# Kernel tuning notes

Hardware: AMD Instinct MI355X
Metric: run time of the kernel (lower is better)

The kernel has to match this reference:

```python
import jax, jax.numpy as jnp
import numpy as np

N, IN_CH, OUT_CH = 100000, 512, 512


def setup_inputs() -> dict:
    key = jax.random.key(0)
    k1, k2, k3, k4 = jax.random.split(key, 4)
    # Xavier-uniform bounds: sqrt(6/(fan_in+fan_out)); Im uses gain=0.1
    bound = float(np.sqrt(6.0 / (IN_CH + OUT_CH)))
    x_re = jax.random.normal(k1, (N, IN_CH), dtype=jnp.float32)
    x_im = jax.random.normal(k2, (N, IN_CH), dtype=jnp.float32)
    Re = jax.random.uniform(k3, (OUT_CH, IN_CH), dtype=jnp.float32, minval=-bound, maxval=bound)
    Im = jax.random.uniform(k4, (OUT_CH, IN_CH), dtype=jnp.float32, minval=-0.1 * bound, maxval=0.1 * bound)
    return {"x_re": x_re, "x_im": x_im, "Re": Re, "Im": Im}


def reference(x_re, x_im, Re, Im):
    # Complex linear: out = x @ (Re + i*Im)^T, summed over in_channels.
    # Equivalent to torch.sum(x[:,None,:] * W[None,:,:], dim=2) but as GEMMs.
    out_re = jnp.einsum('ni,oi->no', x_re, Re) - jnp.einsum('ni,oi->no', x_im, Im)
    out_im = jnp.einsum('ni,oi->no', x_re, Im) + jnp.einsum('ni,oi->no', x_im, Re)
    return jnp.stack([out_re, out_im])  # (2, N, out_channels): real, imag
```

## Files before the change

### kernel.cpp

```cpp
#include <hip/hip_runtime.h>
#include <hip/hip_bf16.h>
#include <cstdint>

#define NROWS  100000
#define KDIM   1024
#define MPAD   100096
#define MTILES 391
#define NTILES 4
#define NBLK   (MTILES * NTILES)

typedef __attribute__((ext_vector_type(8))) __bf16 bf16x8;
typedef __attribute__((ext_vector_type(4))) float  f32x4;

__device__ __forceinline__ uint16_t f2bf(float f) {
    union { float f; uint32_t u; } v; v.f = f;
    uint32_t u = v.u;
    u += 0x7FFFu + ((u >> 16) & 1u);
    return (uint16_t)(u >> 16);
}

__device__ __forceinline__ void async16(const uint16_t* g, uint16_t* l) {
    __builtin_amdgcn_global_load_lds(
        (const __attribute__((address_space(1))) uint32_t*)g,
        (__attribute__((address_space(3))) uint32_t*)l,
        16, 0, 0);
}

__global__ __launch_bounds__(256) void pack_a_kernel(
        const float* __restrict__ xre, const float* __restrict__ xim,
        uint16_t* __restrict__ A) {
    int c = blockIdx.x * 256 + threadIdx.x;
    int n = c >> 7;
    int j = c & 127;
    uint32_t p0 = 0, p1 = 0, p2 = 0, p3 = 0;
    if (n < NROWS) {
        const float* src = (j < 64) ? (xre + (size_t)n * 512 + (size_t)j * 8)
                                    : (xim + (size_t)n * 512 + (size_t)(j - 64) * 8);
        float4 a = ((const float4*)src)[0];
        float4 b = ((const float4*)src)[1];
        p0 = (uint32_t)f2bf(a.x) | ((uint32_t)f2bf(a.y) << 16);
        p1 = (uint32_t)f2bf(a.z) | ((uint32_t)f2bf(a.w) << 16);
        p2 = (uint32_t)f2bf(b.x) | ((uint32_t)f2bf(b.y) << 16);
        p3 = (uint32_t)f2bf(b.z) | ((uint32_t)f2bf(b.w) << 16);
    }
    uint4 v; v.x = p0; v.y = p1; v.z = p2; v.w = p3;
    *(uint4*)(A + (size_t)c * 8) = v;
}

__global__ __launch_bounds__(256) void pack_b_kernel(
        const float* __restrict__ Re, const float* __restrict__ Im,
        uint16_t* __restrict__ Bt) {
    int c  = blockIdx.x * 256 + threadIdx.x;
    int oc = c >> 7;
    int j  = c & 127;
    const float* src;
    float sgn = 1.0f;
    if (oc < 512) {
        if (j < 64) { src = Re + (size_t)oc * 512 + (size_t)j * 8; }
        else        { src = Im + (size_t)oc * 512 + (size_t)(j - 64) * 8; sgn = -1.0f; }
    } else {
        int o = oc - 512;
        if (j < 64) { src = Im + (size_t)o * 512 + (size_t)j * 8; }
        else        { src = Re + (size_t)o * 512 + (size_t)(j - 64) * 8; }
    }
    float4 a = ((const float4*)src)[0];
    float4 b = ((const float4*)src)[1];
    uint32_t p0 = (uint32_t)f2bf(sgn * a.x) | ((uint32_t)f2bf(sgn * a.y) << 16);
    uint32_t p1 = (uint32_t)f2bf(sgn * a.z) | ((uint32_t)f2bf(sgn * a.w) << 16);
    uint32_t p2 = (uint32_t)f2bf(sgn * b.x) | ((uint32_t)f2bf(sgn * b.y) << 16);
    uint32_t p3 = (uint32_t)f2bf(sgn * b.z) | ((uint32_t)f2bf(sgn * b.w) << 16);
    uint4 v; v.x = p0; v.y = p1; v.z = p2; v.w = p3;
    *(uint4*)(Bt + (size_t)c * 8) = v;
}

__global__ __launch_bounds__(512, 2) void gemm8(
        const uint16_t* __restrict__ A, const uint16_t* __restrict__ Bt,
        float* __restrict__ C) {
    __shared__ uint16_t lds[65536];

    const int t    = threadIdx.x;
    const int wave = t >> 6;
    const int lane = t & 63;
    const int q    = lane >> 4;
    const int r16  = lane & 15;
    const int wm   = wave >> 2;
    const int wn   = wave & 3;

    const int bid  = blockIdx.x;
    const int xcd  = bid & 7, lid = bid >> 3;
    const int wgid = (xcd < 4 ? xcd * 196 : 784 + (xcd - 4) * 195) + lid;
    const int colTile = wgid & 3;
    const int rowTile = wgid >> 2;
    const int aRow0   = rowTile * 256;

    const int s7  = r16 & 7;
    const int sA0 = r16 * 64 + ((q ^ s7) << 3);
    const int sA1 = r16 * 64 + (((q + 4) ^ s7) << 3);

    const int g0 = t, g1 = t + 512;
    const int r0 = g0 >> 3, k0 = ((g0 & 7) ^ (r0 & 7)) << 3;
    const int r1 = g1 >> 3, k1 = ((g1 & 7) ^ (r1 & 7)) << 3;
    const int lA00 = g0 * 8,          lA01 = g1 * 8;
    const int lA10 = 8192 + g0 * 8,   lA11 = 8192 + g1 * 8;
    const int lB00 = 16384 + g0 * 8,  lB01 = 16384 + g1 * 8;
    const int lB10 = 24576 + g0 * 8,  lB11 = 24576 + g1 * 8;
    const uint16_t* pA00 = A  + (size_t)(aRow0 + r0) * KDIM + k0;
    const uint16_t* pA01 = A  + (size_t)(aRow0 + r1) * KDIM + k1;
    const uint16_t* pA10 = A  + (size_t)(aRow0 + 128 + r0) * KDIM + k0;
    const uint16_t* pA11 = A  + (size_t)(aRow0 + 128 + r1) * KDIM + k1;
    const uint16_t* pB00 = Bt + (size_t)(colTile * 256 + r0) * KDIM + k0;
    const uint16_t* pB01 = Bt + (size_t)(colTile * 256 + r1) * KDIM + k1;
    const uint16_t* pB10 = Bt + (size_t)(colTile * 256 + 128 + r0) * KDIM + k0;
    const uint16_t* pB11 = Bt + (size_t)(colTile * 256 + 128 + r1) * KDIM + k1;

    async16(pA00, lds + lA00); async16(pA01, lds + lA01);
    async16(pA10, lds + lA10); async16(pA11, lds + lA11);
    async16(pB00, lds + lB00); async16(pB01, lds + lB01);
    async16(pB10, lds + lB10); async16(pB11, lds + lB11);
    async16(pA00 + 64, lds + 32768 + lA00); async16(pA01 + 64, lds + 32768 + lA01);
    async16(pA10 + 64, lds + 32768 + lA10); async16(pA11 + 64, lds + 32768 + lA11);
    async16(pB00 + 64, lds + 32768 + lB00); async16(pB01 + 64, lds + 32768 + lB01);
    async16(pB10 + 64, lds + 32768 + lB10); async16(pB11 + 64, lds + 32768 + lB11);
    pA00 += 128; pA01 += 128; pA10 += 128; pA11 += 128;
    pB00 += 128; pB01 += 128; pB10 += 128; pB11 += 128;
    asm volatile("s_waitcnt vmcnt(8)" ::: "memory");
    __builtin_amdgcn_s_barrier();

    f32x4 acc[8][4] = {};

#pragma unroll 2
    for (int kt = 0; kt < 16; ++kt) {
        const int bufO = (kt & 1) << 15;
        const uint16_t* bA = lds + bufO + wm * 8192;
        const uint16_t* bB = lds + bufO + 16384 + (wn >> 1) * 8192 + (wn & 1) * 4096;
        uint16_t* ldsd = lds + bufO;

        bf16x8 af[4][2], b0[2][2], b1[2][2];
#pragma unroll
        for (int mi = 0; mi < 4; ++mi) {
            af[mi][0] = *(const bf16x8*)(bA + mi * 1024 + sA0);
            af[mi][1] = *(const bf16x8*)(bA + mi * 1024 + sA1);
        }
#pragma unroll
        for (int ni = 0; ni < 2; ++ni) {
            b0[ni][0] = *(const bf16x8*)(bB + ni * 1024 + sA0);
            b0[ni][1] = *(const bf16x8*)(bB + ni * 1024 + sA1);
        }
        __builtin_amdgcn_s_barrier();
        __builtin_amdgcn_s_setprio(1);
#pragma unroll
        for (int mi = 0; mi < 4; ++mi)
#pragma unroll
            for (int nj = 0; nj < 2; ++nj) {
                acc[mi][nj] = __builtin_amdgcn_mfma_f32_16x16x32_bf16(af[mi][0], b0[nj][0], acc[mi][nj], 0, 0, 0);
                acc[mi][nj] = __builtin_amdgcn_mfma_f32_16x16x32_bf16(af[mi][1], b0[nj][1], acc[mi][nj], 0, 0, 0);
            }
        __builtin_amdgcn_s_setprio(0);
        __builtin_amdgcn_s_barrier();
#pragma unroll
        for (int ni = 0; ni < 2; ++ni) {
            b1[ni][0] = *(const bf16x8*)(bB + 2048 + ni * 1024 + sA0);
            b1[ni][1] = *(const bf16x8*)(bB + 2048 + ni * 1024 + sA1);
        }
        __builtin_amdgcn_s_barrier();
        __builtin_amdgcn_s_setprio(1);
#pragma unroll
        for (int mi = 0; mi < 4; ++mi)
#pragma unroll
            for (int nj = 0; nj < 2; ++nj) {
                acc[mi][2 + nj] = __builtin_amdgcn_mfma_f32_16x16x32_bf16(af[mi][0], b1[nj][0], acc[mi][2 + nj], 0, 0, 0);
                acc[mi][2 + nj] = __builtin_amdgcn_mfma_f32_16x16x32_bf16(af[mi][1], b1[nj][1], acc[mi][2 + nj], 0, 0, 0);
            }
        __builtin_amdgcn_s_setprio(0);
        __builtin_amdgcn_s_barrier();
#pragma unroll
        for (int mi = 0; mi < 4; ++mi) {
            af[mi][0] = *(const bf16x8*)(bA + 4096 + mi * 1024 + sA0);
            af[mi][1] = *(const bf16x8*)(bA + 4096 + mi * 1024 + sA1);
        }
        if (kt < 14) {
            __builtin_amdgcn_sched_barrier(0);
            async16(pB00, ldsd + lB00); async16(pB01, ldsd + lB01);
            async16(pB10, ldsd + lB10); async16(pB11, ldsd + lB11);
        }
        __builtin_amdgcn_s_barrier();
        __builtin_amdgcn_s_setprio(1);
#pragma unroll
        for (int mi = 0; mi < 4; ++mi)
#pragma unroll
            for (int nj = 0; nj < 2; ++nj) {
                acc[4 + mi][2 + nj] = __builtin_amdgcn_mfma_f32_16x16x32_bf16(af[mi][0], b1[nj][0], acc[4 + mi][2 + nj], 0, 0, 0);
                acc[4 + mi][2 + nj] = __builtin_amdgcn_mfma_f32_16x16x32_bf16(af[mi][1], b1[nj][1], acc[4 + mi][2 + nj], 0, 0, 0);
            }
        __builtin_amdgcn_s_setprio(0);
        __builtin_amdgcn_s_barrier();
        if (kt < 14) {
            __builtin_amdgcn_sched_barrier(0);
            async16(pA00, ldsd + lA00); async16(pA01, ldsd + lA01);
            async16(pA10, ldsd + lA10); async16(pA11, ldsd + lA11);
            pA00 += 64; pA01 += 64; pA10 += 64; pA11 += 64;
            pB00 += 64; pB01 += 64; pB10 += 64; pB11 += 64;
        }
        __builtin_amdgcn_s_barrier();
        __builtin_amdgcn_s_setprio(1);
#pragma unroll
        for (int mi = 0; mi < 4; ++mi)
#pragma unroll
            for (int nj = 0; nj < 2; ++nj) {
                acc[4 + mi][nj] = __builtin_amdgcn_mfma_f32_16x16x32_bf16(af[mi][0], b0[nj][0], acc[4 + mi][nj], 0, 0, 0);
                acc[4 + mi][nj] = __builtin_amdgcn_mfma_f32_16x16x32_bf16(af[mi][1], b0[nj][1], acc[4 + mi][nj], 0, 0, 0);
            }
        __builtin_amdgcn_s_setprio(0);
        if (kt < 14)       asm volatile("s_waitcnt vmcnt(8)" ::: "memory");
        else if (kt == 14) asm volatile("s_waitcnt vmcnt(0)" ::: "memory");
        __builtin_amdgcn_s_barrier();
    }

    const size_t outHalf = (colTile >= 2) ? (size_t)NROWS * 512 : 0;
    const int cb = (colTile & 1) * 256 + wn * 64;
#pragma unroll
    for (int mi8 = 0; mi8 < 8; ++mi8) {
        int rbase = aRow0 + wm * 128 + mi8 * 16 + q * 4;
#pragma unroll
        for (int nj = 0; nj < 4; ++nj) {
            int col = cb + nj * 16 + r16;
#pragma unroll
            for (int r = 0; r < 4; ++r) {
                int row = rbase + r;
                if (row < NROWS)
                    C[outHalf + (size_t)row * 512 + col] = acc[mi8][nj][r];
            }
        }
    }
}

__global__ void fallback_kernel(const float* __restrict__ xre,
                                const float* __restrict__ xim,
                                const float* __restrict__ Re,
                                const float* __restrict__ Im,
                                float* __restrict__ out) {
    __shared__ float sre[512], sim[512];
    int n = blockIdx.x;
    for (int i = threadIdx.x; i < 512; i += 256) {
        sre[i] = xre[(size_t)n * 512 + i];
        sim[i] = xim[(size_t)n * 512 + i];
    }
    __syncthreads();
    for (int o = threadIdx.x; o < 512; o += 256) {
        float are = 0.f, aim = 0.f;
        for (int k = 0; k < 512; ++k) {
            float wr = Re[(size_t)o * 512 + k], wi = Im[(size_t)o * 512 + k];
            float xr = sre[k], xi = sim[k];
            are += xr * wr - xi * wi;
            aim += xr * wi + xi * wr;
        }
        out[(size_t)n * 512 + o] = are;
        out[(size_t)NROWS * 512 + (size_t)n * 512 + o] = aim;
    }
}

extern "C" void kernel_launch(void* const* d_in, const int* in_sizes, int n_in,
                              void* d_out, int out_size, void* d_ws, size_t ws_size,
                              hipStream_t stream) {
    const float* xre = (const float*)d_in[0];
    const float* xim = (const float*)d_in[1];
    const float* Re  = (const float*)d_in[2];
    const float* Im  = (const float*)d_in[3];
    float* out = (float*)d_out;

    const size_t aBytes = (size_t)MPAD * KDIM * 2;
    const size_t bBytes = (size_t)1024 * KDIM * 2;
    if (ws_size >= aBytes + bBytes) {
        uint16_t* A  = (uint16_t*)d_ws;
        uint16_t* Bt = (uint16_t*)((char*)d_ws + aBytes);
        pack_a_kernel<<<(MPAD * 128) / 256, 256, 0, stream>>>(xre, xim, A);
        pack_b_kernel<<<(1024 * 128) / 256, 256, 0, stream>>>(Re, Im, Bt);
        gemm8<<<NBLK, 512, 0, stream>>>(A, Bt, out);
    } else {
        fallback_kernel<<<NROWS, 256, 0, stream>>>(xre, xim, Re, Im, out);
    }
}
```

Baseline: 867.3 us.

## Fuse fp32-to-bf16 activation conversion into GEMM, dropping the separate pack kernel

Result: faster. 816.4 us (-5.9%).

```diff
diff --git a/kernel.cpp b/kernel.cpp
--- a/kernel.cpp
+++ b/kernel.cpp
@@ -4,7 +4,6 @@
 
 #define NROWS  100000
 #define KDIM   1024
-#define MPAD   100096
 #define MTILES 391
 #define NTILES 4
 #define NBLK   (MTILES * NTILES)
@@ -19,6 +18,12 @@
     return (uint16_t)(u >> 16);
 }
 
+__device__ __forceinline__ uint32_t pkbf(float lo, float hi) {
+    uint32_t r;
+    asm("v_cvt_pk_bf16_f32 %0, %1, %2" : "=v"(r) : "v"(lo), "v"(hi));
+    return r;
+}
+
 __device__ __forceinline__ void async16(const uint16_t* g, uint16_t* l) {
     __builtin_amdgcn_global_load_lds(
         (const __attribute__((address_space(1))) uint32_t*)g,
@@ -26,25 +31,16 @@
         16, 0, 0);
 }
 
-__global__ __launch_bounds__(256) void pack_a_kernel(
-        const float* __restrict__ xre, const float* __restrict__ xim,
-        uint16_t* __restrict__ A) {
-    int c = blockIdx.x * 256 + threadIdx.x;
-    int n = c >> 7;
-    int j = c & 127;
-    uint32_t p0 = 0, p1 = 0, p2 = 0, p3 = 0;
-    if (n < NROWS) {
-        const float* src = (j < 64) ? (xre + (size_t)n * 512 + (size_t)j * 8)
-                                    : (xim + (size_t)n * 512 + (size_t)(j - 64) * 8);
-        float4 a = ((const float4*)src)[0];
-        float4 b = ((const float4*)src)[1];
-        p0 = (uint32_t)f2bf(a.x) | ((uint32_t)f2bf(a.y) << 16);
-        p1 = (uint32_t)f2bf(a.z) | ((uint32_t)f2bf(a.w) << 16);
-        p2 = (uint32_t)f2bf(b.x) | ((uint32_t)f2bf(b.y) << 16);
-        p3 = (uint32_t)f2bf(b.z) | ((uint32_t)f2bf(b.w) << 16);
-    }
-    uint4 v; v.x = p0; v.y = p1; v.z = p2; v.w = p3;
-    *(uint4*)(A + (size_t)c * 8) = v;
+__device__ __forceinline__ void ldA(const float* p, bool ok, float4& a, float4& b) {
+    if (ok) { a = ((const float4*)p)[0]; b = ((const float4*)p)[1]; }
+    else    { a = make_float4(0.f,0.f,0.f,0.f); b = make_float4(0.f,0.f,0.f,0.f); }
+}
+
+__device__ __forceinline__ void wrA(uint16_t* d, float4 a, float4 b) {
+    uint4 u;
+    u.x = pkbf(a.x, a.y); u.y = pkbf(a.z, a.w);
+    u.z = pkbf(b.x, b.y); u.w = pkbf(b.z, b.w);
+    *(uint4*)d = u;
 }
 
 __global__ __launch_bounds__(256) void pack_b_kernel(
@@ -74,8 +70,8 @@
 }
 
 __global__ __launch_bounds__(512, 2) void gemm8(
-        const uint16_t* __restrict__ A, const uint16_t* __restrict__ Bt,
-        float* __restrict__ C) {
+        const float* __restrict__ xre, const float* __restrict__ xim,
+        const uint16_t* __restrict__ Bt, float* __restrict__ C) {
     __shared__ uint16_t lds[65536];
 
     const int t    = threadIdx.x;
@@ -97,138 +93,166 @@
     const int sA0 = r16 * 64 + ((q ^ s7) << 3);
     const int sA1 = r16 * 64 + (((q + 4) ^ s7) << 3);
 
-    const int g0 = t, g1 = t + 512;
-    const int r0 = g0 >> 3, k0 = ((g0 & 7) ^ (r0 & 7)) << 3;
-    const int r1 = g1 >> 3, k1 = ((g1 & 7) ^ (r1 & 7)) << 3;
-    const int lA00 = g0 * 8,          lA01 = g1 * 8;
-    const int lA10 = 8192 + g0 * 8,   lA11 = 8192 + g1 * 8;
-    const int lB00 = 16384 + g0 * 8,  lB01 = 16384 + g1 * 8;
-    const int lB10 = 24576 + g0 * 8,  lB11 = 24576 + g1 * 8;
-    const uint16_t* pA00 = A  + (size_t)(aRow0 + r0) * KDIM + k0;
-    const uint16_t* pA01 = A  + (size_t)(aRow0 + r1) * KDIM + k1;
-    const uint16_t* pA10 = A  + (size_t)(aRow0 + 128 + r0) * KDIM + k0;
-    const uint16_t* pA11 = A  + (size_t)(aRow0 + 128 + r1) * KDIM + k1;
-    const uint16_t* pB00 = Bt + (size_t)(colTile * 256 + r0) * KDIM + k0;
-    const uint16_t* pB01 = Bt + (size_t)(colTile * 256 + r1) * KDIM + k1;
-    const uint16_t* pB10 = Bt + (size_t)(colTile * 256 + 128 + r0) * KDIM + k0;
-    const uint16_t* pB11 = Bt + (size_t)(colTile * 256 + 128 + r1) * KDIM + k1;
-
-    async16(pA00, lds + lA00); async16(pA01, lds + lA01);
-    async16(pA10, lds + lA10); async16(pA11, lds + lA11);
-    async16(pB00, lds + lB00); async16(pB01, lds + lB01);
-    async16(pB10, lds + lB10); async16(pB11, lds + lB11);
-    async16(pA00 + 64, lds + 32768 + lA00); async16(pA01 + 64, lds + 32768 + lA01);
-    async16(pA10 + 64, lds + 32768 + lA10); async16(pA11 + 64, lds + 32768 + lA11);
-    async16(pB00 + 64, lds + 32768 + lB00); async16(pB01 + 64, lds + 32768 + lB01);
-    async16(pB10 + 64, lds + 32768 + lB10); async16(pB11 + 64, lds + 32768 + lB11);
-    pA00 += 128; pA01 += 128; pA10 += 128; pA11 += 128;
-    pB00 += 128; pB01 += 128; pB10 += 128; pB11 += 128;
-    asm volatile("s_waitcnt vmcnt(8)" ::: "memory");
-    __builtin_amdgcn_s_barrier();
+    const int r0 = t >> 3;
+    const int kc = ((t & 7) ^ (r0 & 7)) << 3;
+    const int lA0 = t * 8;
+    const int lA1 = 4096 + t * 8;
+    const int lA2 = 8192 + t * 8;
+    const int lA3 = 12288 + t * 8;
+    const size_t base = (size_t)(aRow0 + r0) * 512 + kc;
+    const size_t off0 = base;
+    const size_t off1 = base + (size_t)64  * 512;
+    const size_t off2 = base + (size_t)128 * 512;
+    const size_t off3 = base + (size_t)192 * 512;
+    const bool ok0 = aRow0 + r0       < NROWS;
+    const bool ok1 = aRow0 + 64 + r0  < NROWS;
+    const bool ok2 = aRow0 + 128 + r0 < NROWS;
+    const bool ok3 = aRow0 + 192 + r0 < NROWS;
+    const int lB0 = 16384 + t * 8, lB1 = 20480 + t * 8;
+    const int lB2 = 24576 + t * 8, lB3 = 28672 + t * 8;
+    const uint16_t* pB0 = Bt + (size_t)(colTile * 256 + r0)       * KDIM + kc;
+    const uint16_t* pB1 = Bt + (size_t)(colTile * 256 + 64 + r0)  * KDIM + kc;
+    const uint16_t* pB2 = Bt + (size_t)(colTile * 256 + 128 + r0) * KDIM + kc;
+    const uint16_t* pB3 = Bt + (size_t)(colTile * 256 + 192 + r0) * KDIM + kc;
+
+    {
+        float4 a0, b0, a1, b1;
+        ldA(xre + off0, ok0, a0, b0);
+        ldA(xre + off2, ok2, a1, b1);
+        async16(pB0, lds + lB0); async16(pB1, lds + lB1);
+        async16(pB2, lds + lB2); async16(pB3, lds + lB3);
+        async16(pB0 + 64, lds + 32768 + lB0); async16(pB1 + 64, lds + 32768 + lB1);
+        async16(pB2 + 64, lds + 32768 + lB2); async16(pB3 + 64, lds + 32768 + lB3);
+        wrA(lds + lA0, a0, b0); wrA(lds + lA2, a1, b1);
+        ldA(xre + off1, ok1, a0, b0);
+        ldA(xre + off3, ok3, a1, b1);
+        wrA(lds + lA1, a0, b0); wrA(lds + lA3, a1, b1);
+        asm volatile("s_waitcnt lgkmcnt(0)" ::: "memory");
+        __builtin_amdgcn_s_barrier();
+    }
 
     f32x4 acc[8][4] = {};
+    float4 x0a, x0b, x1a, x1b;
 
 #pragma unroll 2
     for (int kt = 0; kt < 16; ++kt) {
         const int bufO = (kt & 1) << 15;
         const uint16_t* bA = lds + bufO + wm * 8192;
-        const uint16_t* bB = lds + bufO + 16384 + (wn >> 1) * 8192 + (wn & 1) * 4096;
-        uint16_t* ldsd = lds + bufO;
-
-        bf16x8 af[4][2], b0[2][2], b1[2][2];
-#pragma unroll
-        for (int mi = 0; mi < 4; ++mi) {
-            af[mi][0] = *(const bf16x8*)(bA + mi * 1024 + sA0);
-            af[mi][1] = *(const bf16x8*)(bA + mi * 1024 + sA1);
-        }
-#pragma unroll
-        for (int ni = 0; ni < 2; ++ni) {
-            b0[ni][0] = *(const bf16x8*)(bB + ni * 1024 + sA0);
-            b0[ni][1] = *(const bf16x8*)(bB + ni * 1024 + sA1);
-        }
+        const uint16_t* bB = lds + bufO + 16384 + wn * 4096;
+        uint16_t* AdC = lds + bufO;
+        uint16_t* AdN = lds + (bufO ^ 32768);
+        const float* srcN = (kt + 1 < 8) ? xre : xim;
+        const float* spN  = srcN + ((kt + 1) & 7) * 64;
+
+        bf16x8 af[4], bfr[4];
+        if (kt > 0) {
+            wrA(AdC + lA1, x0a, x0b); wrA(AdC + lA3, x1a, x1b);
+        }
+        if (kt < 15) {
+            ldA(spN + off0, ok0, x0a, x0b);
+            ldA(spN + off2, ok2, x1a, x1b);
+            __builtin_amdgcn_sched_barrier(0);
+        }
+#pragma unroll
+        for (int mi = 0; mi < 4; ++mi)
+            af[mi] = *(const bf16x8*)(bA + mi * 1024 + sA0);
+#pragma unroll
+        for (int nj = 0; nj < 4; ++nj)
+            bfr[nj] = *(const bf16x8*)(bB + nj * 1024 + sA0);
+        asm volatile("s_waitcnt lgkmcnt(0)" ::: "memory");
         __builtin_amdgcn_s_barrier();
         __builtin_amdgcn_s_setprio(1);
 #pragma unroll
         for (int mi = 0; mi < 4; ++mi)
 #pragma unroll
-            for (int nj = 0; nj < 2; ++nj) {
-                acc[mi][nj] = __builtin_amdgcn_mfma_f32_16x16x32_bf16(af[mi][0], b0[nj][0], acc[mi][nj], 0, 0, 0);
-                acc[mi][nj] = __builtin_amdgcn_mfma_f32_16x16x32_bf16(af[mi][1], b0[nj][1], acc[mi][nj], 0, 0, 0);
-            }
+            for (int nj = 0; nj < 4; ++nj)
+                acc[mi][nj] = __builtin_amdgcn_mfma_f32_16x16x32_bf16(
+                    af[mi], bfr[nj], acc[mi][nj], 0, 0, 0);
         __builtin_amdgcn_s_setprio(0);
         __builtin_amdgcn_s_barrier();
 #pragma unroll
-        for (int ni = 0; ni < 2; ++ni) {
-            b1[ni][0] = *(const bf16x8*)(bB + 2048 + ni * 1024 + sA0);
-            b1[ni][1] = *(const bf16x8*)(bB + 2048 + ni * 1024 + sA1);
-        }
+        for (int mi = 0; mi < 4; ++mi)
+            af[mi] = *(const bf16x8*)(bA + 4096 + mi * 1024 + sA0);
         __builtin_amdgcn_s_barrier();
         __builtin_amdgcn_s_setprio(1);
 #pragma unroll
         for (int mi = 0; mi < 4; ++mi)
 #pragma unroll
-            for (int nj = 0; nj < 2; ++nj) {
-                acc[mi][2 + nj] = __builtin_amdgcn_mfma_f32_16x16x32_bf16(af[mi][0], b1[nj][0], acc[mi][2 + nj], 0, 0, 0);
-                acc[mi][2 + nj] = __builtin_amdgcn_mfma_f32_16x16x32_bf16(af[mi][1], b1[nj][1], acc[mi][2 + nj], 0, 0, 0);
-            }
+            for (int nj = 0; nj < 4; ++nj)
+                acc[4 + mi][nj] = __builtin_amdgcn_mfma_f32_16x16x32_bf16(
+                    af[mi], bfr[nj], acc[4 + mi][nj], 0, 0, 0);
         __builtin_amdgcn_s_setprio(0);
         __builtin_amdgcn_s_barrier();
-#pragma unroll
-        for (int mi = 0; mi < 4; ++mi) {
-            af[mi][0] = *(const bf16x8*)(bA + 4096 + mi * 1024 + sA0);
-            af[mi][1] = *(const bf16x8*)(bA + 4096 + mi * 1024 + sA1);
-        }
+        if (kt < 15) {
+            wrA(AdN + lA0, x0a, x0b); wrA(AdN + lA2, x1a, x1b);
+            ldA(spN + off1, ok1, x0a, x0b);
+            ldA(spN + off3, ok3, x1a, x1b);
+            __builtin_amdgcn_sched_barrier(0);
+        }
+#pragma unroll
+        for (int mi = 0; mi < 4; ++mi)
+            af[mi] = *(const bf16x8*)(bA + 4096 + mi * 1024 + sA1);
+#pragma unroll
+        for (int nj = 0; nj < 4; ++nj)
+            bfr[nj] = *(const bf16x8*)(bB + nj * 1024 + sA1);
+        asm volatile("s_waitcnt lgkmcnt(0)" ::: "memory");
+        __builtin_amdgcn_s_barrier();
+        __builtin_amdgcn_s_setprio(1);
+#pragma unroll
+        for (int mi = 0; mi < 4; ++mi)
+#pragma unroll
+            for (int nj = 0; nj < 4; ++nj)
+                acc[4 + mi][nj] = __builtin_amdgcn_mfma_f32_16x16x32_bf16(
+                    af[mi], bfr[nj], acc[4 + mi][nj], 0, 0, 0);
+        __builtin_amdgcn_s_setprio(0);
+        __builtin_amdgcn_s_barrier();
         if (kt < 14) {
-            __builtin_amdgcn_sched_barrier(0);
-            async16(pB00, ldsd + lB00); async16(pB01, ldsd + lB01);
-            async16(pB10, ldsd + lB10); async16(pB11, ldsd + lB11);
-        }
+            const size_t gk = (size_t)(kt + 2) * 64;
+            async16(pB0 + gk, lds + bufO + lB0); async16(pB1 + gk, lds + bufO + lB1);
+            async16(pB2 + gk, lds + bufO + lB2); async16(pB3 + gk, lds + bufO + lB3);
+        }
+#pragma unroll
+        for (int mi = 0; mi < 4; ++mi)
+            af[mi] = *(const bf16x8*)(bA + mi * 1024 + sA1);
         __builtin_amdgcn_s_barrier();
         __builtin_amdgcn_s_setprio(1);
 #pragma unroll
         for (int mi = 0; mi < 4; ++mi)
 #pragma unroll
-            for (int nj = 0; nj < 2; ++nj) {
-                acc[4 + mi][2 + nj] = __builtin_amdgcn_mfma_f32_16x16x32_bf16(af[mi][0], b1[nj][0], acc[4 + mi][2 + nj], 0, 0, 0);
-                acc[4 + mi][2 + nj] = __builtin_amdgcn_mfma_f32_16x16x32_bf16(af[mi][1], b1[nj][1], acc[4 + mi][2 + nj], 0, 0, 0);
-            }
+            for (int nj = 0; nj < 4; ++nj)
+                acc[mi][nj] = __builtin_amdgcn_mfma_f32_16x16x32_bf16(
+                    af[mi], bfr[nj], acc[mi][nj], 0, 0, 0);
         __builtin_amdgcn_s_setprio(0);
-        __builtin_amdgcn_s_barrier();
-        if (kt < 14) {
-            __builtin_amdgcn_sched_barrier(0);
-            async16(pA00, ldsd + lA00); async16(pA01, ldsd + lA01);
-            async16(pA10, ldsd + lA10); async16(pA11, ldsd + lA11);
-            pA00 += 64; pA01 += 64; pA10 += 64; pA11 += 64;
-            pB00 += 64; pB01 += 64; pB10 += 64; pB11 += 64;
-        }
-        __builtin_amdgcn_s_barrier();
-        __builtin_amdgcn_s_setprio(1);
-#pragma unroll
-        for (int mi = 0; mi < 4; ++mi)
-#pragma unroll
-            for (int nj = 0; nj < 2; ++nj) {
-                acc[4 + mi][nj] = __builtin_amdgcn_mfma_f32_16x16x32_bf16(af[mi][0], b0[nj][0], acc[4 + mi][nj], 0, 0, 0);
-                acc[4 + mi][nj] = __builtin_amdgcn_mfma_f32_16x16x32_bf16(af[mi][1], b0[nj][1], acc[4 + mi][nj], 0, 0, 0);
-            }
-        __builtin_amdgcn_s_setprio(0);
-        if (kt < 14)       asm volatile("s_waitcnt vmcnt(8)" ::: "memory");
-        else if (kt == 14) asm volatile("s_waitcnt vmcnt(0)" ::: "memory");
         __builtin_amdgcn_s_barrier();
     }
 
     const size_t outHalf = (colTile >= 2) ? (size_t)NROWS * 512 : 0;
     const int cb = (colTile & 1) * 256 + wn * 64;
-#pragma unroll
-    for (int mi8 = 0; mi8 < 8; ++mi8) {
-        int rbase = aRow0 + wm * 128 + mi8 * 16 + q * 4;
-#pragma unroll
-        for (int nj = 0; nj < 4; ++nj) {
-            int col = cb + nj * 16 + r16;
-#pragma unroll
-            for (int r = 0; r < 4; ++r) {
-                int row = rbase + r;
-                if (row < NROWS)
-                    C[outHalf + (size_t)row * 512 + col] = acc[mi8][nj][r];
+    if (aRow0 + 256 <= NROWS) {
+#pragma unroll
+        for (int mi8 = 0; mi8 < 8; ++mi8) {
+            int rbase = aRow0 + wm * 128 + mi8 * 16 + q * 4;
+#pragma unroll
+            for (int nj = 0; nj < 4; ++nj) {
+                int col = cb + nj * 16 + r16;
+#pragma unroll
+                for (int r = 0; r < 4; ++r)
+                    C[outHalf + (size_t)(rbase + r) * 512 + col] = acc[mi8][nj][r];
+            }
+        }
+    } else {
+#pragma unroll
+        for (int mi8 = 0; mi8 < 8; ++mi8) {
+            int rbase = aRow0 + wm * 128 + mi8 * 16 + q * 4;
+#pragma unroll
+            for (int nj = 0; nj < 4; ++nj) {
+                int col = cb + nj * 16 + r16;
+#pragma unroll
+                for (int r = 0; r < 4; ++r) {
+                    int row = rbase + r;
+                    if (row < NROWS)
+                        C[outHalf + (size_t)row * 512 + col] = acc[mi8][nj][r];
+                }
             }
         }
     }
@@ -268,14 +292,11 @@
     const float* Im  = (const float*)d_in[3];
     float* out = (float*)d_out;
 
-    const size_t aBytes = (size_t)MPAD * KDIM * 2;
     const size_t bBytes = (size_t)1024 * KDIM * 2;
-    if (ws_size >= aBytes + bBytes) {
-        uint16_t* A  = (uint16_t*)d_ws;
-        uint16_t* Bt = (uint16_t*)((char*)d_ws + aBytes);
-        pack_a_kernel<<<(MPAD * 128) / 256, 256, 0, stream>>>(xre, xim, A);
+    if (ws_size >= bBytes) {
+        uint16_t* Bt = (uint16_t*)d_ws;
         pack_b_kernel<<<(1024 * 128) / 256, 256, 0, stream>>>(Re, Im, Bt);
-        gemm8<<<NBLK, 512, 0, stream>>>(A, Bt, out);
+        gemm8<<<NBLK, 512, 0, stream>>>(xre, xim, Bt, out);
     } else {
         fallback_kernel<<<NROWS, 256, 0, stream>>>(xre, xim, Re, Im, out);
     }
```
